# Optimization experiments

Measured on AMD Instinct MI355X. Metric: run time of the kernel, lower is better.

Reference implementation:

```python
import jax, jax.numpy as jnp
import numpy as np

N = 100000      # nodes
E = 1600000     # edges (avg degree 16)
DIN, H, DOUT = 256, 256, 64
THETA1, THETA2, LAMDA = 0.1, 0.5, 1.0


def setup_inputs() -> dict:
    key = jax.random.key(0)
    ks = jax.random.split(key, 16)
    inp = {}
    inp["x"] = jax.random.normal(ks[0], (N, DIN), jnp.float32)
    inp["A_idx"] = jax.random.randint(ks[1], (2, E), 0, N)
    inp["A_val"] = jax.random.uniform(ks[2], (E,), jnp.float32) / 16.0  # ~normalized adjacency
    inp["L_idx"] = jax.random.randint(ks[3], (2, E), 0, N)
    inp["L_val"] = jax.random.normal(ks[4], (E,), jnp.float32) * 0.05   # Laplacian entries
    dims = [DIN, H, DOUT]
    k = 5
    for i in range(2):
        din, dh = dims[i], dims[i + 1]
        inp[f"gcn_w{i}"] = jax.random.normal(ks[k], (din, dh), jnp.float32) / np.sqrt(din).astype(np.float32); k += 1
        inp[f"gcn_b{i}"] = jnp.zeros((dh,), jnp.float32)
        inp[f"pai1_{i}"] = jax.random.normal(ks[k], (dh, dh), jnp.float32) * 0.05; k += 1
        inp[f"pai2_{i}"] = jax.random.normal(ks[k], (DIN, dh), jnp.float32) * 0.05; k += 1
        inp[f"w1_w{i}"] = jax.random.normal(ks[k], (dh, DOUT), jnp.float32) / np.sqrt(dh).astype(np.float32); k += 1
        inp[f"w1_b{i}"] = jnp.zeros((DOUT,), jnp.float32)
        inp[f"w2_w{i}"] = jax.random.normal(ks[k], (dh, DOUT), jnp.float32) / np.sqrt(dh).astype(np.float32); k += 1
        inp[f"w2_b{i}"] = jnp.zeros((DOUT,), jnp.float32)
    return inp


def _spmm(idx, val, X):
    # sparse (COO) @ dense: out[r] += val_e * X[c] for each edge e=(r,c)
    return jax.ops.segment_sum(val[:, None] * X[idx[1]], idx[0], num_segments=N)


def _activation(x):
    # piecewise multi-term ReLU activation from Net.activation
    w1 = (2.0 * THETA2 - THETA1) / THETA2
    w2 = w1 - 1.0
    def soft(t):
        return jax.nn.relu(x - t) - jax.nn.relu(-x - t)
    return w1 * soft(THETA1) - w2 * soft(THETA2)


def _forward(x, A_idx, A_val, L_idx, L_val, params):
    X = x
    Z_tp = x
    z_tp_list, z_embed_list = [], []
    for (gcn_w, gcn_b, pai1, pai2, w1_w, w1_b, w2_w, w2_b) in params:
        # GCN layer: A @ (Z W) + b, then ReLU  (dropout = identity in eval mode)
        Z_tp = jax.nn.relu(_spmm(A_idx, A_val, Z_tp @ gcn_w) + gcn_b)
        z_tp_list.append(jnp.tanh(Z_tp @ w1_w + w1_b))
        # embedding update: Z pai1 + X pai2 - lamda * L @ Z, custom activation
        Z_embed = Z_tp @ pai1 + X @ pai2 - LAMDA * _spmm(L_idx, L_val, Z_tp)
        Z_embed = _activation(Z_embed)
        z_embed_list.append(jnp.tanh(Z_embed @ w2_w + w2_b))
        Z_tp = Z_embed
    return (z_tp_list[0], z_tp_list[1], z_embed_list[0], z_embed_list[1])


def reference(x, A_idx, A_val, L_idx, L_val,
              gcn_w0, gcn_b0, pai1_0, pai2_0, w1_w0, w1_b0, w2_w0, w2_b0,
              gcn_w1, gcn_b1, pai1_1, pai2_1, w1_w1, w1_b1, w2_w1, w2_b1):
    params = [
        (gcn_w0, gcn_b0, pai1_0, pai2_0, w1_w0, w1_b0, w2_w0, w2_b0),
        (gcn_w1, gcn_b1, pai1_1, pai2_1, w1_w1, w1_b1, w2_w1, w2_b1),
    ]
    return _forward(x, A_idx, A_val, L_idx, L_val, params)
```

## Files before the change

kernel.cpp:

```cpp
#include <hip/hip_runtime.h>
#include <hip/hip_bf16.h>
#include <stdint.h>

static constexpr int N_NODES = 100000;
static constexpr int N_EDGES = 1600000;
static constexpr int PAD_ROWS = 100096;

static constexpr int CB_SHIFT = 9;
static constexpr int CRPB = 1 << CB_SHIFT;
static constexpr int NCB = 196;
static constexpr int CCAP = 8960;
static constexpr int CHUNK = 4096;

typedef _Float16 f16;
using f16x8 = __attribute__((ext_vector_type(8))) _Float16;
using f16x4v = __attribute__((ext_vector_type(4))) _Float16;
using f32x4 = __attribute__((ext_vector_type(4))) float;

__device__ __forceinline__ void gld_lds16(const void* g, void* l) {
  __builtin_amdgcn_global_load_lds((const __attribute__((address_space(1))) void*)g,
                                   (__attribute__((address_space(3))) void*)l, 16, 0, 0);
}

__device__ __forceinline__ float custom_act(float x) {
  float s1 = fmaxf(x - 0.1f, 0.f) - fmaxf(-x - 0.1f, 0.f);
  float s2 = fmaxf(x - 0.5f, 0.f) - fmaxf(-x - 0.5f, 0.f);
  return 1.8f * s1 - 0.8f * s2;
}

__global__ __launch_bounds__(256) void xconv_k(const float* __restrict__ src, f16* __restrict__ dst, int n4) {
  int i = blockIdx.x * 256 + threadIdx.x;
  if (i < n4) {
    float4 v = ((const float4*)src)[i];
    f16x4v h = {(f16)v.x, (f16)v.y, (f16)v.z, (f16)v.w};
    ((f16x4v*)dst)[i] = h;
  }
}
__global__ __launch_bounds__(256) void wconv_k(const float* __restrict__ src, f16* __restrict__ dst, int K, int N) {
  int i = blockIdx.x * 256 + threadIdx.x;
  if (i < K * N) { int k = i / N, n = i - k * N; dst[n * K + k] = (f16)src[i]; }
}

__global__ __launch_bounds__(256) void part_k(const int* __restrict__ Ai, const float* __restrict__ Av,
                                              int* __restrict__ bcA, int2* __restrict__ bufA,
                                              const int* __restrict__ Li, const float* __restrict__ Lv,
                                              int* __restrict__ bcL, int2* __restrict__ bufL, int E) {
  __shared__ int histA[NCB], histL[NCB];
  __shared__ int baseA[NCB], baseL[NCB];
  int tid = threadIdx.x;
  int e0 = blockIdx.x * CHUNK;
  int e1 = min(e0 + CHUNK, E);
  for (int i = tid; i < NCB; i += 256) { histA[i] = 0; histL[i] = 0; }
  __syncthreads();
  for (int e = e0 + tid; e < e1; e += 256) {
    atomicAdd(&histA[Ai[e] >> CB_SHIFT], 1);
    atomicAdd(&histL[Li[e] >> CB_SHIFT], 1);
  }
  __syncthreads();
  if (tid < NCB) {
    int hA = histA[tid], hL = histL[tid];
    baseA[tid] = hA ? atomicAdd(&bcA[tid * 16], hA) : 0;
    baseL[tid] = hL ? atomicAdd(&bcL[tid * 16], hL) : 0;
    histA[tid] = 0;
    histL[tid] = 0;
  }
  __syncthreads();
  for (int e = e0 + tid; e < e1; e += 256) {
    {
      int r = Ai[e], c = Ai[E + e];
      int b = r >> CB_SHIFT;
      int p = baseA[b] + atomicAdd(&histA[b], 1);
      if (p < CCAP) bufA[(size_t)b * CCAP + p] = make_int2(((r & (CRPB - 1)) << 17) | c, __float_as_int(Av[e]));
    }
    {
      int r = Li[e], c = Li[E + e];
      int b = r >> CB_SHIFT;
      int p = baseL[b] + atomicAdd(&histL[b], 1);
      if (p < CCAP) bufL[(size_t)b * CCAP + p] = make_int2(((r & (CRPB - 1)) << 17) | c, __float_as_int(Lv[e]));
    }
  }
}

__global__ __launch_bounds__(1024) void scan_k(const int* __restrict__ cntA, int* __restrict__ rpA,
                                               const int* __restrict__ cntL, int* __restrict__ rpL,
                                               int n, int stride) {
  const int* cnt = blockIdx.x ? cntL : cntA;
  int* rp = blockIdx.x ? rpL : rpA;
  __shared__ int wsum[16];
  __shared__ int carry_s;
  int tid = threadIdx.x, lane = tid & 63, wv = tid >> 6;
  if (tid == 0) carry_s = 0;
  __syncthreads();
  for (int base = 0; base < n; base += 1024) {
    int i = base + tid;
    int v = (i < n) ? cnt[i * stride] : 0;
    int s = v;
    #pragma unroll
    for (int off = 1; off < 64; off <<= 1) {
      int t = __shfl_up(s, off, 64);
      if (lane >= off) s += t;
    }
    if (lane == 63) wsum[wv] = s;
    __syncthreads();
    if (wv == 0 && lane < 16) {
      int w = wsum[lane];
      #pragma unroll
      for (int off = 1; off < 16; off <<= 1) {
        int t = __shfl_up(w, off, 64);
        if (lane >= off) w += t;
      }
      wsum[lane] = w;
    }
    __syncthreads();
    int carry = carry_s;
    int woff = wv ? wsum[wv - 1] : 0;
    if (i < n) rp[i] = carry + woff + s - v;
    __syncthreads();
    if (tid == 1023) carry_s = carry + woff + s;
    __syncthreads();
  }
  if (tid == 0) rp[n] = carry_s;
}

__global__ __launch_bounds__(256) void place_k(const int* __restrict__ bcA, const int* __restrict__ bbA,
                                               const int2* __restrict__ bufA, int* __restrict__ rpA,
                                               int2* __restrict__ recA,
                                               const int* __restrict__ bcL, const int* __restrict__ bbL,
                                               const int2* __restrict__ bufL, int* __restrict__ rpL,
                                               int2* __restrict__ recL) {
  const int b = blockIdx.x;
  const int* bc; const int* bb; const int2* buf; int* rp; int2* rec;
  if (blockIdx.y) { bc = bcL; bb = bbL; buf = bufL; rp = rpL; rec = recL; }
  else            { bc = bcA; bb = bbA; buf = bufA; rp = rpA; rec = recA; }
  __shared__ int lcnt[CRPB];
  __shared__ int wsum[4];
  int tid = threadIdx.x, lane = tid & 63, wv = tid >> 6;
  int nrec = min(bc[b * 16], CCAP);
  const int2* src = buf + (size_t)b * CCAP;
  lcnt[2 * tid] = 0;
  lcnt[2 * tid + 1] = 0;
  __syncthreads();
  for (int i = tid; i < nrec; i += 256) atomicAdd(&lcnt[src[i].x >> 17], 1);
  __syncthreads();
  int c0 = lcnt[2 * tid], c1 = lcnt[2 * tid + 1];
  int s = c0 + c1;
  int incl = s;
  #pragma unroll
  for (int off = 1; off < 64; off <<= 1) {
    int t = __shfl_up(incl, off, 64);
    if (lane >= off) incl += t;
  }
  if (lane == 63) wsum[wv] = incl;
  __syncthreads();
  int woff = 0;
  for (int w = 0; w < wv; ++w) woff += wsum[w];
  int base0 = bb[b] + woff + incl - s;
  int base1 = base0 + c0;
  __syncthreads();
  lcnt[2 * tid] = base0;
  lcnt[2 * tid + 1] = base1;
  rp[b * CRPB + 2 * tid] = base0;
  rp[b * CRPB + 2 * tid + 1] = base1;
  __syncthreads();
  for (int i = tid; i < nrec; i += 256) {
    int2 r = src[i];
    int pos = atomicAdd(&lcnt[r.x >> 17], 1);
    rec[pos] = make_int2(r.x & 0x1FFFF, r.y);
  }
}

template<int VEC>
__global__ __launch_bounds__(256) void spmm_k(const int* __restrict__ rp, const int2* __restrict__ rec,
                                              const f16* __restrict__ X,
                                              const f16* __restrict__ base, const float* __restrict__ bias,
                                              f16* __restrict__ out, int mode, int nrows) {
  int lane = threadIdx.x & 63;
  int row = blockIdx.x * 4 + (threadIdx.x >> 6);
  if (row >= nrows) return;
  const int M = VEC * 64;
  int p0 = __builtin_amdgcn_readfirstlane(rp[row]);
  int p1 = __builtin_amdgcn_readfirstlane(rp[row + 1]);
  float acc[VEC] = {};
  int p = p0;
  for (; p + 7 < p1; p += 8) {
    int2 e[8];
    #pragma unroll
    for (int u = 0; u < 8; ++u) e[u] = rec[p + u];
    if (VEC == 4) {
      f16x4v xv[8];
      #pragma unroll
      for (int u = 0; u < 8; ++u) xv[u] = *(const f16x4v*)(X + (size_t)e[u].x * M + lane * 4);
      #pragma unroll
      for (int u = 0; u < 8; ++u) {
        float v = __int_as_float(e[u].y);
        #pragma unroll
        for (int j = 0; j < 4; ++j) acc[j] += v * (float)xv[u][j];
      }
    } else {
      float xv[8];
      #pragma unroll
      for (int u = 0; u < 8; ++u) xv[u] = (float)X[(size_t)e[u].x * M + lane];
      #pragma unroll
      for (int u = 0; u < 8; ++u) acc[0] += __int_as_float(e[u].y) * xv[u];
    }
  }
  for (; p + 1 < p1; p += 2) {
    int2 e0 = rec[p], e1 = rec[p + 1];
    float v0 = __int_as_float(e0.y), v1 = __int_as_float(e1.y);
    if (VEC == 4) {
      f16x4v x0 = *(const f16x4v*)(X + (size_t)e0.x * M + lane * 4);
      f16x4v x1 = *(const f16x4v*)(X + (size_t)e1.x * M + lane * 4);
      #pragma unroll
      for (int j = 0; j < 4; ++j) acc[j] += v0 * (float)x0[j] + v1 * (float)x1[j];
    } else {
      float x0 = (float)X[(size_t)e0.x * M + lane];
      float x1 = (float)X[(size_t)e1.x * M + lane];
      acc[0] += v0 * x0 + v1 * x1;
    }
  }
  if (p < p1) {
    int2 e0 = rec[p];
    float v0 = __int_as_float(e0.y);
    if (VEC == 4) {
      f16x4v x0 = *(const f16x4v*)(X + (size_t)e0.x * M + lane * 4);
      #pragma unroll
      for (int j = 0; j < 4; ++j) acc[j] += v0 * (float)x0[j];
    } else {
      acc[0] += v0 * (float)X[(size_t)e0.x * M + lane];
    }
  }
  size_t o = (size_t)row * M + (size_t)lane * VEC;
  if (VEC == 4) {
    f16x4v r;
    if (mode == 0) {
      #pragma unroll
      for (int j = 0; j < 4; ++j) r[j] = (f16)fmaxf(acc[j] + bias[lane * 4 + j], 0.f);
    } else {
      f16x4v bv = *(const f16x4v*)(base + o);
      #pragma unroll
      for (int j = 0; j < 4; ++j) r[j] = (f16)custom_act((float)bv[j] - acc[j]);
    }
    *(f16x4v*)(out + o) = r;
  } else {
    if (mode == 0) out[o] = (f16)fmaxf(acc[0] + bias[lane], 0.f);
    else out[o] = (f16)custom_act((float)base[o] - acc[0]);
  }
}

template<int BN>
__global__ __launch_bounds__(256) void gemm_k(const f16* __restrict__ A1, int K1,
                                              const f16* __restrict__ A2, int K2,
                                              const f16* __restrict__ B1t, const f16* __restrict__ B2t,
                                              const float* __restrict__ bias,
                                              void* __restrict__ C, int cf16, int epi,
                                              int nrows, int ldc) {
  __shared__ f16 As[128 * 32];
  __shared__ f16 Bs[BN * 32];
  int tid = threadIdx.x, lane = tid & 63, wv = tid >> 6;
  int m16 = lane & 15, quad = lane >> 4;
  int r0 = blockIdx.x * 128, c0 = blockIdx.y * BN;
  int wr0 = wv * 32;
  f32x4 acc[2][BN / 16] = {};
  int srow = lane >> 2, scol = (lane & 3) * 8;
  for (int src = 0; src < 2; ++src) {
    const f16* A = src ? A2 : A1;
    if (!A) continue;
    int K = src ? K2 : K1;
    const f16* Bt = src ? B2t : B1t;
    const f16* gA = A + (size_t)(r0 + wr0 + srow) * K + scol;
    const f16* gB = (BN == 128) ? Bt + (size_t)(c0 + wr0 + srow) * K + scol
                                : Bt + (size_t)(c0 + wv * 16 + srow) * K + scol;
    f16* lA = &As[wr0 * 32];
    f16* lB = (BN == 128) ? &Bs[wr0 * 32] : &Bs[wv * 16 * 32];
    for (int k0 = 0; k0 < K; k0 += 32) {
      gld_lds16(gA + k0, lA);
      gld_lds16(gA + k0 + (size_t)16 * K, lA + 512);
      gld_lds16(gB + k0, lB);
      if (BN == 128) gld_lds16(gB + k0 + (size_t)16 * K, lB + 512);
      __syncthreads();
      f16x8 a0 = *(const f16x8*)&As[(wr0 + m16) * 32 + quad * 8];
      f16x8 a1 = *(const f16x8*)&As[(wr0 + 16 + m16) * 32 + quad * 8];
      #pragma unroll
      for (int bt = 0; bt < BN / 16; ++bt) {
        f16x8 b = *(const f16x8*)&Bs[(bt * 16 + m16) * 32 + quad * 8];
        acc[0][bt] = __builtin_amdgcn_mfma_f32_16x16x32_f16(a0, b, acc[0][bt], 0, 0, 0);
        acc[1][bt] = __builtin_amdgcn_mfma_f32_16x16x32_f16(a1, b, acc[1][bt], 0, 0, 0);
      }
      __syncthreads();
    }
  }
  #pragma unroll
  for (int rt = 0; rt < 2; ++rt) {
    #pragma unroll
    for (int bt = 0; bt < BN / 16; ++bt) {
      #pragma unroll
      for (int j = 0; j < 4; ++j) {
        int row = r0 + wr0 + rt * 16 + quad * 4 + j;
        if (row >= nrows) continue;
        int colp = c0 + bt * 16 + m16;
        float v = acc[rt][bt][j];
        if (bias) v += bias[colp];
        if (epi == 1) v = tanhf(v);
        size_t o = (size_t)row * ldc + colp;
        if (cf16) ((f16*)C)[o] = (f16)v;
        else ((float*)C)[o] = v;
      }
    }
  }
}

extern "C" void kernel_launch(void* const* d_in, const int* in_sizes, int n_in,
                              void* d_out, int out_size, void* d_ws, size_t ws_size,
                              hipStream_t stream) {
  const float* x  = (const float*)d_in[0];
  const int*   Ai = (const int*)d_in[1];
  const float* Av = (const float*)d_in[2];
  const int*   Li = (const int*)d_in[3];
  const float* Lv = (const float*)d_in[4];
  const float* gcn_w0 = (const float*)d_in[5];
  const float* gcn_b0 = (const float*)d_in[6];
  const float* pai1_0 = (const float*)d_in[7];
  const float* pai2_0 = (const float*)d_in[8];
  const float* w1_w0  = (const float*)d_in[9];
  const float* w1_b0  = (const float*)d_in[10];
  const float* w2_w0  = (const float*)d_in[11];
  const float* w2_b0  = (const float*)d_in[12];
  const float* gcn_w1 = (const float*)d_in[13];
  const float* gcn_b1 = (const float*)d_in[14];
  const float* pai1_1 = (const float*)d_in[15];
  const float* pai2_1 = (const float*)d_in[16];
  const float* w1_w1  = (const float*)d_in[17];
  const float* w1_b1  = (const float*)d_in[18];
  const float* w2_w1  = (const float*)d_in[19];
  const float* w2_b1  = (const float*)d_in[20];
  float* out = (float*)d_out;

  const int N = N_NODES, E = N_EDGES;
  const size_t PH = (size_t)PAD_ROWS * 256;
  const size_t Pd = (size_t)PAD_ROWS * 64;
  const size_t Nd = (size_t)N * 64;

  f16* xh  = (f16*)d_ws;
  f16* R1  = xh + PH;
  f16* R2  = R1 + PH;
  f16* wts = R2 + PH;
  f16* gcn_w0t = wts;
  f16* pai1_0t = gcn_w0t + 65536;
  f16* pai2_0t = pai1_0t + 65536;
  f16* w1_w0t  = pai2_0t + 65536;
  f16* w2_w0t  = w1_w0t + 16384;
  f16* gcn_w1t = w2_w0t + 16384;
  f16* pai2_1t = gcn_w1t + 16384;
  f16* pai1_1t = pai2_1t + 16384;
  f16* w1_w1t  = pai1_1t + 4096;
  f16* w2_w1t  = w1_w1t + 4096;
  int2* recA = (int2*)(((uintptr_t)(w2_w1t + 4096) + 255) & ~(uintptr_t)255);
  int2* recL = recA + E;
  int*  rpA  = (int*)(recL + E);
  int*  rpL  = rpA + (PAD_ROWS + 512);
  int*  bcA  = rpL + (PAD_ROWS + 512);
  int*  bcL  = bcA + NCB * 16;
  int*  bbA  = bcL + NCB * 16;
  int*  bbL  = bbA + (NCB + 1);

  int2* bufA = (int2*)R1;
  int2* bufL = bufA + (size_t)NCB * CCAP;

  f16* T1h   = R2;
  f16* Ztp1h = R2 + Pd;
  f16* Z1bh  = R2 + 2 * Pd;

  xconv_k<<<(int)(((size_t)N * 64 + 255) / 256), 256, 0, stream>>>(x, xh, N * 64);
  wconv_k<<<(65536 + 255) / 256, 256, 0, stream>>>(gcn_w0, gcn_w0t, 256, 256);
  wconv_k<<<(65536 + 255) / 256, 256, 0, stream>>>(pai1_0, pai1_0t, 256, 256);
  wconv_k<<<(65536 + 255) / 256, 256, 0, stream>>>(pai2_0, pai2_0t, 256, 256);
  wconv_k<<<(16384 + 255) / 256, 256, 0, stream>>>(w1_w0, w1_w0t, 256, 64);
  wconv_k<<<(16384 + 255) / 256, 256, 0, stream>>>(w2_w0, w2_w0t, 256, 64);
  wconv_k<<<(16384 + 255) / 256, 256, 0, stream>>>(gcn_w1, gcn_w1t, 256, 64);
  wconv_k<<<(16384 + 255) / 256, 256, 0, stream>>>(pai2_1, pai2_1t, 256, 64);
  wconv_k<<<(4096 + 255) / 256, 256, 0, stream>>>(pai1_1, pai1_1t, 64, 64);
  wconv_k<<<(4096 + 255) / 256, 256, 0, stream>>>(w1_w1, w1_w1t, 64, 64);
  wconv_k<<<(4096 + 255) / 256, 256, 0, stream>>>(w2_w1, w2_w1t, 64, 64);

  hipMemsetAsync(bcA, 0, sizeof(int) * (size_t)NCB * 16 * 2, stream);
  part_k<<<(E + CHUNK - 1) / CHUNK, 256, 0, stream>>>(Ai, Av, bcA, bufA, Li, Lv, bcL, bufL, E);
  scan_k<<<2, 1024, 0, stream>>>(bcA, bbA, bcL, bbL, NCB, 16);
  place_k<<<dim3(NCB, 2), 256, 0, stream>>>(bcA, bbA, bufA, rpA, recA,
                                            bcL, bbL, bufL, rpL, recL);

  const int MB = PAD_ROWS / 128;
  dim3 g256(MB, 2), g64(MB, 1);
  const int spmm_grid = (N + 3) / 4;

  gemm_k<128><<<g256, 256, 0, stream>>>(xh, 256, nullptr, 0, gcn_w0t, nullptr, nullptr, R1, 1, 0, N, 256);
  spmm_k<4><<<spmm_grid, 256, 0, stream>>>(rpA, recA, R1, nullptr, gcn_b0, R2, 0, N);
  gemm_k<64><<<g64, 256, 0, stream>>>(R2, 256, nullptr, 0, w1_w0t, nullptr, w1_b0, out, 0, 1, N, 64);
  gemm_k<128><<<g256, 256, 0, stream>>>(R2, 256, xh, 256, pai1_0t, pai2_0t, nullptr, R1, 1, 0, N, 256);
  spmm_k<4><<<spmm_grid, 256, 0, stream>>>(rpL, recL, R2, R1, nullptr, R1, 1, N);
  gemm_k<64><<<g64, 256, 0, stream>>>(R1, 256, nullptr, 0, w2_w0t, nullptr, w2_b0, out + 2 * Nd, 0, 1, N, 64);

  gemm_k<64><<<g64, 256, 0, stream>>>(R1, 256, nullptr, 0, gcn_w1t, nullptr, nullptr, T1h, 1, 0, N, 64);
  spmm_k<1><<<spmm_grid, 256, 0, stream>>>(rpA, recA, T1h, nullptr, gcn_b1, Ztp1h, 0, N);
  gemm_k<64><<<g64, 256, 0, stream>>>(Ztp1h, 64, nullptr, 0, w1_w1t, nullptr, w1_b1, out + Nd, 0, 1, N, 64);
  gemm_k<64><<<g64, 256, 0, stream>>>(Ztp1h, 64, xh, 256, pai1_1t, pai2_1t, nullptr, Z1bh, 1, 0, N, 64);
  spmm_k<1><<<spmm_grid, 256, 0, stream>>>(rpL, recL, Ztp1h, Z1bh, nullptr, Z1bh, 1, N);
  gemm_k<64><<<g64, 256, 0, stream>>>(Z1bh, 64, nullptr, 0, w2_w1t, nullptr, w2_b1, out + 3 * Nd, 0, 1, N, 64);
}
```

Before: 898.0 us.

## Batch independent GEMMs into grouped launches, widen K tile with swizzled LDS

The ten weight-conversion launches become one kernel driven by an offset table. Independent GEMMs that read the same input are grouped into a single launch, with blockIdx.y selecting the job, which cuts launch count and lets small 64-column GEMMs run alongside larger ones. The GEMM K step grows from 32 to 64 with an XOR-swizzled LDS layout to reduce bank conflicts and halve the number of barriers. In exchange, shared memory rises to 32KB per block and BN becomes a runtime value, so the epilogue loop and accumulator sizing are no longer compile-time specialised, which may raise register use.

```diff
diff --git a/kernel.cpp b/kernel.cpp
--- a/kernel.cpp
+++ b/kernel.cpp
@@ -36,9 +36,21 @@
     ((f16x4v*)dst)[i] = h;
   }
 }
-__global__ __launch_bounds__(256) void wconv_k(const float* __restrict__ src, f16* __restrict__ dst, int K, int N) {
+
+struct WC {
+  const float* src[10];
+  f16* dst[10];
+  int K[10], N[10], beg[11];
+};
+__global__ __launch_bounds__(256) void wconv_k(WC wc) {
   int i = blockIdx.x * 256 + threadIdx.x;
-  if (i < K * N) { int k = i / N, n = i - k * N; dst[n * K + k] = (f16)src[i]; }
+  if (i >= wc.beg[10]) return;
+  int s = 0;
+  while (s < 9 && i >= wc.beg[s + 1]) ++s;
+  int local = i - wc.beg[s];
+  int N = wc.N[s];
+  int k = local / N, n = local - k * N;
+  wc.dst[s][n * wc.K[s] + k] = (f16)wc.src[s][local];
 }
 
 __global__ __launch_bounds__(256) void part_k(const int* __restrict__ Ai, const float* __restrict__ Av,
@@ -247,58 +259,83 @@
   }
 }
 
-template<int BN>
-__global__ __launch_bounds__(256) void gemm_k(const f16* __restrict__ A1, int K1,
-                                              const f16* __restrict__ A2, int K2,
-                                              const f16* __restrict__ B1t, const f16* __restrict__ B2t,
-                                              const float* __restrict__ bias,
-                                              void* __restrict__ C, int cf16, int epi,
-                                              int nrows, int ldc) {
-  __shared__ f16 As[128 * 32];
-  __shared__ f16 Bs[BN * 32];
+struct GJobs {
+  const f16* A1[3]; const f16* A2[3];
+  const f16* B1[3]; const f16* B2[3];
+  const float* bias[3];
+  void* C[3];
+  int K1[3], K2[3], cf16[3], epi[3], ldc[3], bn[3], c0[3];
+};
+
+__global__ __launch_bounds__(256) void gemm_k(GJobs jb, int nrows) {
+  __shared__ f16 As[128 * 64];
+  __shared__ f16 Bs[128 * 64];
+  const int j = blockIdx.y;
+  const int BN = jb.bn[j], c0 = jb.c0[j], ldc = jb.ldc[j];
+  const int nbt = BN >> 4;
   int tid = threadIdx.x, lane = tid & 63, wv = tid >> 6;
   int m16 = lane & 15, quad = lane >> 4;
-  int r0 = blockIdx.x * 128, c0 = blockIdx.y * BN;
+  int r0 = blockIdx.x * 128;
   int wr0 = wv * 32;
-  f32x4 acc[2][BN / 16] = {};
-  int srow = lane >> 2, scol = (lane & 3) * 8;
+  f32x4 acc[2][8] = {};
+  int srow = lane >> 3;
+  int sg = (lane & 7) ^ (srow & 7);
+  int bRows = (BN == 128) ? 32 : 16;
+  int aswz = (m16 & 7) * 8;
   for (int src = 0; src < 2; ++src) {
-    const f16* A = src ? A2 : A1;
+    const f16* A = src ? jb.A2[j] : jb.A1[j];
     if (!A) continue;
-    int K = src ? K2 : K1;
-    const f16* Bt = src ? B2t : B1t;
-    const f16* gA = A + (size_t)(r0 + wr0 + srow) * K + scol;
-    const f16* gB = (BN == 128) ? Bt + (size_t)(c0 + wr0 + srow) * K + scol
-                                : Bt + (size_t)(c0 + wv * 16 + srow) * K + scol;
-    f16* lA = &As[wr0 * 32];
-    f16* lB = (BN == 128) ? &Bs[wr0 * 32] : &Bs[wv * 16 * 32];
-    for (int k0 = 0; k0 < K; k0 += 32) {
-      gld_lds16(gA + k0, lA);
-      gld_lds16(gA + k0 + (size_t)16 * K, lA + 512);
+    int K = src ? jb.K2[j] : jb.K1[j];
+    const f16* Bt = src ? jb.B2[j] : jb.B1[j];
+    const f16* gA = A + (size_t)(r0 + wr0 + srow) * K + sg * 8;
+    const f16* gB = Bt + (size_t)(c0 + wv * bRows + srow) * K + sg * 8;
+    f16* lA = &As[wr0 * 64];
+    f16* lB = &Bs[wv * bRows * 64];
+    for (int k0 = 0; k0 < K; k0 += 64) {
+      #pragma unroll
+      for (int c = 0; c < 4; ++c) gld_lds16(gA + k0 + (size_t)(c * 8) * K, lA + c * 512);
       gld_lds16(gB + k0, lB);
-      if (BN == 128) gld_lds16(gB + k0 + (size_t)16 * K, lB + 512);
-      __syncthreads();
-      f16x8 a0 = *(const f16x8*)&As[(wr0 + m16) * 32 + quad * 8];
-      f16x8 a1 = *(const f16x8*)&As[(wr0 + 16 + m16) * 32 + quad * 8];
-      #pragma unroll
-      for (int bt = 0; bt < BN / 16; ++bt) {
-        f16x8 b = *(const f16x8*)&Bs[(bt * 16 + m16) * 32 + quad * 8];
-        acc[0][bt] = __builtin_amdgcn_mfma_f32_16x16x32_f16(a0, b, acc[0][bt], 0, 0, 0);
-        acc[1][bt] = __builtin_amdgcn_mfma_f32_16x16x32_f16(a1, b, acc[1][bt], 0, 0, 0);
+      gld_lds16(gB + k0 + (size_t)8 * K, lB + 512);
+      if (BN == 128) {
+        gld_lds16(gB + k0 + (size_t)16 * K, lB + 1024);
+        gld_lds16(gB + k0 + (size_t)24 * K, lB + 1536);
       }
       __syncthreads();
-    }
-  }
-  #pragma unroll
+      #pragma unroll
+      for (int ks = 0; ks < 2; ++ks) {
+        int gsl = ((ks * 4 + quad) * 8) ^ aswz;
+        f16x8 a0 = *(const f16x8*)&As[(wr0 + m16) * 64 + gsl];
+        f16x8 a1 = *(const f16x8*)&As[(wr0 + 16 + m16) * 64 + gsl];
+        if (BN == 128) {
+          #pragma unroll
+          for (int bt = 0; bt < 8; ++bt) {
+            f16x8 b = *(const f16x8*)&Bs[(bt * 16 + m16) * 64 + gsl];
+            acc[0][bt] = __builtin_amdgcn_mfma_f32_16x16x32_f16(a0, b, acc[0][bt], 0, 0, 0);
+            acc[1][bt] = __builtin_amdgcn_mfma_f32_16x16x32_f16(a1, b, acc[1][bt], 0, 0, 0);
+          }
+        } else {
+          #pragma unroll
+          for (int bt = 0; bt < 4; ++bt) {
+            f16x8 b = *(const f16x8*)&Bs[(bt * 16 + m16) * 64 + gsl];
+            acc[0][bt] = __builtin_amdgcn_mfma_f32_16x16x32_f16(a0, b, acc[0][bt], 0, 0, 0);
+            acc[1][bt] = __builtin_amdgcn_mfma_f32_16x16x32_f16(a1, b, acc[1][bt], 0, 0, 0);
+          }
+        }
+      }
+      __syncthreads();
+    }
+  }
+  const float* bias = jb.bias[j];
+  int cf16 = jb.cf16[j], epi = jb.epi[j];
+  void* C = jb.C[j];
   for (int rt = 0; rt < 2; ++rt) {
-    #pragma unroll
-    for (int bt = 0; bt < BN / 16; ++bt) {
-      #pragma unroll
-      for (int j = 0; j < 4; ++j) {
-        int row = r0 + wr0 + rt * 16 + quad * 4 + j;
+    for (int bt = 0; bt < nbt; ++bt) {
+      #pragma unroll
+      for (int jj = 0; jj < 4; ++jj) {
+        int row = r0 + wr0 + rt * 16 + quad * 4 + jj;
         if (row >= nrows) continue;
         int colp = c0 + bt * 16 + m16;
-        float v = acc[rt][bt][j];
+        float v = acc[rt][bt][jj];
         if (bias) v += bias[colp];
         if (epi == 1) v = tanhf(v);
         size_t o = (size_t)row * ldc + colp;
@@ -371,16 +408,20 @@
   f16* Z1bh  = R2 + 2 * Pd;
 
   xconv_k<<<(int)(((size_t)N * 64 + 255) / 256), 256, 0, stream>>>(x, xh, N * 64);
-  wconv_k<<<(65536 + 255) / 256, 256, 0, stream>>>(gcn_w0, gcn_w0t, 256, 256);
-  wconv_k<<<(65536 + 255) / 256, 256, 0, stream>>>(pai1_0, pai1_0t, 256, 256);
-  wconv_k<<<(65536 + 255) / 256, 256, 0, stream>>>(pai2_0, pai2_0t, 256, 256);
-  wconv_k<<<(16384 + 255) / 256, 256, 0, stream>>>(w1_w0, w1_w0t, 256, 64);
-  wconv_k<<<(16384 + 255) / 256, 256, 0, stream>>>(w2_w0, w2_w0t, 256, 64);
-  wconv_k<<<(16384 + 255) / 256, 256, 0, stream>>>(gcn_w1, gcn_w1t, 256, 64);
-  wconv_k<<<(16384 + 255) / 256, 256, 0, stream>>>(pai2_1, pai2_1t, 256, 64);
-  wconv_k<<<(4096 + 255) / 256, 256, 0, stream>>>(pai1_1, pai1_1t, 64, 64);
-  wconv_k<<<(4096 + 255) / 256, 256, 0, stream>>>(w1_w1, w1_w1t, 64, 64);
-  wconv_k<<<(4096 + 255) / 256, 256, 0, stream>>>(w2_w1, w2_w1t, 64, 64);
+  {
+    WC wc;
+    const float* s[10] = {gcn_w0, pai1_0, pai2_0, w1_w0, w2_w0, gcn_w1, pai2_1, pai1_1, w1_w1, w2_w1};
+    f16* d[10] = {gcn_w0t, pai1_0t, pai2_0t, w1_w0t, w2_w0t, gcn_w1t, pai2_1t, pai1_1t, w1_w1t, w2_w1t};
+    int K[10] = {256, 256, 256, 256, 256, 256, 256, 64, 64, 64};
+    int Nn[10] = {256, 256, 256, 64, 64, 64, 64, 64, 64, 64};
+    int off = 0;
+    for (int i = 0; i < 10; ++i) {
+      wc.src[i] = s[i]; wc.dst[i] = d[i]; wc.K[i] = K[i]; wc.N[i] = Nn[i];
+      wc.beg[i] = off; off += K[i] * Nn[i];
+    }
+    wc.beg[10] = off;
+    wconv_k<<<(off + 255) / 256, 256, 0, stream>>>(wc);
+  }
 
   hipMemsetAsync(bcA, 0, sizeof(int) * (size_t)NCB * 16 * 2, stream);
   part_k<<<(E + CHUNK - 1) / CHUNK, 256, 0, stream>>>(Ai, Av, bcA, bufA, Li, Lv, bcL, bufL, E);
@@ -389,20 +430,49 @@
                                             bcL, bbL, bufL, rpL, recL);
 
   const int MB = PAD_ROWS / 128;
-  dim3 g256(MB, 2), g64(MB, 1);
   const int spmm_grid = (N + 3) / 4;
 
-  gemm_k<128><<<g256, 256, 0, stream>>>(xh, 256, nullptr, 0, gcn_w0t, nullptr, nullptr, R1, 1, 0, N, 256);
+  auto setj = [](GJobs& g, int j, const f16* A1, int K1, const f16* A2, int K2,
+                 const f16* B1, const f16* B2, const float* bias, void* C,
+                 int cf16, int epi, int ldc, int bn, int c0) {
+    g.A1[j] = A1; g.A2[j] = A2; g.B1[j] = B1; g.B2[j] = B2; g.bias[j] = bias; g.C[j] = C;
+    g.K1[j] = K1; g.K2[j] = K2; g.cf16[j] = cf16; g.epi[j] = epi; g.ldc[j] = ldc;
+    g.bn[j] = bn; g.c0[j] = c0;
+  };
+
+  {
+    GJobs g{};
+    setj(g, 0, xh, 256, nullptr, 0, gcn_w0t, nullptr, nullptr, R1, 1, 0, 256, 128, 0);
+    setj(g, 1, xh, 256, nullptr, 0, gcn_w0t, nullptr, nullptr, R1, 1, 0, 256, 128, 128);
+    gemm_k<<<dim3(MB, 2), 256, 0, stream>>>(g, N);
+  }
   spmm_k<4><<<spmm_grid, 256, 0, stream>>>(rpA, recA, R1, nullptr, gcn_b0, R2, 0, N);
-  gemm_k<64><<<g64, 256, 0, stream>>>(R2, 256, nullptr, 0, w1_w0t, nullptr, w1_b0, out, 0, 1, N, 64);
-  gemm_k<128><<<g256, 256, 0, stream>>>(R2, 256, xh, 256, pai1_0t, pai2_0t, nullptr, R1, 1, 0, N, 256);
+  {
+    GJobs g{};
+    setj(g, 0, R2, 256, xh, 256, pai1_0t, pai2_0t, nullptr, R1, 1, 0, 256, 128, 0);
+    setj(g, 1, R2, 256, xh, 256, pai1_0t, pai2_0t, nullptr, R1, 1, 0, 256, 128, 128);
+    setj(g, 2, R2, 256, nullptr, 0, w1_w0t, nullptr, w1_b0, out, 0, 1, 64, 64, 0);
+    gemm_k<<<dim3(MB, 3), 256, 0, stream>>>(g, N);
+  }
   spmm_k<4><<<spmm_grid, 256, 0, stream>>>(rpL, recL, R2, R1, nullptr, R1, 1, N);
-  gemm_k<64><<<g64, 256, 0, stream>>>(R1, 256, nullptr, 0, w2_w0t, nullptr, w2_b0, out + 2 * Nd, 0, 1, N, 64);
-
-  gemm_k<64><<<g64, 256, 0, stream>>>(R1, 256, nullptr, 0, gcn_w1t, nullptr, nullptr, T1h, 1, 0, N, 64);
+  {
+    GJobs g{};
+    setj(g, 0, R1, 256, nullptr, 0, gcn_w1t, nullptr, nullptr, T1h, 1, 0, 64, 64, 0);
+    setj(g, 1, R1, 256, nullptr, 0, w2_w0t, nullptr, w2_b0, out + 2 * Nd, 0, 1, 64, 64, 0);
+    gemm_k<<<dim3(MB, 2), 256, 0, stream>>>(g, N);
+  }
+
   spmm_k<1><<<spmm_grid, 256, 0, stream>>>(rpA, recA, T1h, nullptr, gcn_b1, Ztp1h, 0, N);
-  gemm_k<64><<<g64, 256, 0, stream>>>(Ztp1h, 64, nullptr, 0, w1_w1t, nullptr, w1_b1, out + Nd, 0, 1, N, 64);
-  gemm_k<64><<<g64, 256, 0, stream>>>(Ztp1h, 64, xh, 256, pai1_1t, pai2_1t, nullptr, Z1bh, 1, 0, N, 64);
+  {
+    GJobs g{};
+    setj(g, 0, Ztp1h, 64, xh, 256, pai1_1t, pai2_1t, nullptr, Z1bh, 1, 0, 64, 64, 0);
+    setj(g, 1, Ztp1h, 64, nullptr, 0, w1_w1t, nullptr, w1_b1, out + Nd, 0, 1, 64, 64, 0);
+    gemm_k<<<dim3(MB, 2), 256, 0, stream>>>(g, N);
+  }
   spmm_k<1><<<spmm_grid, 256, 0, stream>>>(rpL, recL, Ztp1h, Z1bh, nullptr, Z1bh, 1, N);
-  gemm_k<64><<<g64, 256, 0, stream>>>(Z1bh, 64, nullptr, 0, w2_w1t, nullptr, w2_b1, out + 3 * Nd, 0, 1, N, 64);
-}
+  {
+    GJobs g{};
+    setj(g, 0, Z1bh, 64, nullptr, 0, w2_w1t, nullptr, w2_b1, out + 3 * Nd, 0, 1, 64, 64, 0);
+    gemm_k<<<dim3(MB, 1), 256, 0, stream>>>(g, N);
+  }
+}
```

Measured after the change: 1.641 ms. 1.83x slower.
